# Optimization experiments

Hardware: AMD Instinct MI355X
Metric: run time of the kernel (lower is better)

The kernel has to match this reference:

```python
import jax, jax.numpy as jnp
import numpy as np


def setup_inputs() -> dict:
    key = jax.random.key(0)
    k1, k2, k3, k4, k5 = jax.random.split(key, 5)
    B, N, M, K, D, O = 4, 32768, 8192, 16, 64, 64
    x = jax.random.normal(k1, (B, N, D), jnp.float32)
    x_subset = jax.random.normal(k2, (B, M, D), jnp.float32)
    knn_index = jax.random.randint(k3, (B, M, K), 0, N, jnp.int32)
    # 1x1 Conv2d(2*D -> O) == per-point linear: weight (O, 2D), bias (O,)
    W = jax.random.normal(k4, (O, 2 * D), jnp.float32) * (1.0 / np.sqrt(2 * D))
    b = jax.random.normal(k5, (O,), jnp.float32) * 0.01
    return {"x": x, "x_subset": x_subset, "knn_index": knn_index, "W": W, "b": b}


def reference(x, x_subset, knn_index, W, b):
    # knn_gather: (B,N,D) indexed by (B,M,K) -> (B,M,K,D)
    grouped = jax.vmap(lambda xb, ib: xb[ib])(x, knn_index)
    center = x_subset[:, :, None, :]                      # (B,M,1,D)
    edge = jnp.concatenate(
        [grouped - center, jnp.broadcast_to(center, grouped.shape)], axis=-1
    )                                                     # (B,M,K,2D)
    # 1x1 conv over channel dim + ReLU, output layout (B,O,M,K)
    h = jax.nn.relu(jnp.einsum("bmkc,oc->bomk", edge, W) + b[None, :, None, None])
    return jnp.max(h, axis=-1)                            # (B,O,M)
```

## Files before the change

kernel.cpp:

```cpp
#include <hip/hip_runtime.h>
#include <math.h>

#define B_ 4
#define N_ 32768
#define M_ 8192
#define K_ 16
#define D_ 64
#define O_ 64

typedef __attribute__((ext_vector_type(8))) short bf16x8;
typedef __attribute__((ext_vector_type(4))) float f32x4;

static __device__ __forceinline__ short f2bf(float f) {
    unsigned u = __float_as_uint(f);
    u += 0x7fffu + ((u >> 16) & 1u);
    return (short)(u >> 16);
}

static __device__ __forceinline__ bf16x8 cvt_bf8(float4 f0, float4 f1) {
    bf16x8 v;
    v[0] = f2bf(f0.x); v[1] = f2bf(f0.y); v[2] = f2bf(f0.z); v[3] = f2bf(f0.w);
    v[4] = f2bf(f1.x); v[5] = f2bf(f1.y); v[6] = f2bf(f1.z); v[7] = f2bf(f1.w);
    return v;
}

static __device__ __forceinline__ bf16x8 ld_bf8(const float* p) {
    return cvt_bf8(*(const float4*)p, *(const float4*)(p + 4));
}

__global__ __launch_bounds__(256, 2)
void fused_gconv(const float* __restrict__ x, const float* __restrict__ xs,
                 const int* __restrict__ idx, const float* __restrict__ W,
                 const float* __restrict__ bias, float* __restrict__ out) {
    __shared__ int    ldsI[64 * 16];
    __shared__ bf16x8 ldsW[4][2][2][64];
    __shared__ float  ldsB[64];
    __shared__ float  ldsT[64 * 65];

    const int tid  = threadIdx.x;
    const int blk  = blockIdx.x;
    const int bb   = blk >> 7;
    const int mblk = (blk & 127) * 64;

    *(int4*)&ldsI[tid * 4] =
        *(const int4*)(idx + ((size_t)bb * M_ + mblk) * 16 + tid * 4);

    const int l  = tid & 63;
    const int wv = tid >> 6;
    const int lr = l & 15;
    const int kg = l >> 4;
    const int mw = wv * 16;

    {
        const int t = wv;
        #pragma unroll
        for (int s = 0; s < 2; ++s) {
            const float* wp = W + (size_t)(t * 16 + lr) * 128 + s * 32 + kg * 8;
            float4 f0 = *(const float4*)wp;
            float4 f1 = *(const float4*)(wp + 4);
            float4 g0 = *(const float4*)(wp + 64);
            float4 g1 = *(const float4*)(wp + 68);
            ldsW[t][s][0][l] = cvt_bf8(f0, f1);
            float4 d0 = make_float4(g0.x - f0.x, g0.y - f0.y, g0.z - f0.z, g0.w - f0.w);
            float4 d1 = make_float4(g1.x - f1.x, g1.y - f1.y, g1.z - f1.z, g1.w - f1.w);
            ldsW[t][s][1][l] = cvt_bf8(d0, d1);
        }
        if (tid < 64) ldsB[tid] = bias[tid];
    }
    __syncthreads();

    bf16x8 b1[2][4];
    float  binit[4];
    #pragma unroll
    for (int t = 0; t < 4; ++t) {
        b1[0][t] = ldsW[t][0][0][l];
        b1[1][t] = ldsW[t][1][0][l];
        binit[t] = ldsB[t * 16 + lr];
    }

    const float* xsp = xs + ((size_t)bb * M_ + mblk + mw + lr) * 64 + kg * 8;
    bf16x8 axs0 = ld_bf8(xsp);
    bf16x8 axs1 = ld_bf8(xsp + 32);

    float vout[4][4];
    #pragma unroll
    for (int t = 0; t < 4; ++t) {
        bf16x8 bd0 = ldsW[t][0][1][l];
        bf16x8 bd1 = ldsW[t][1][1][l];
        f32x4 a = {binit[t], binit[t], binit[t], binit[t]};
        a = __builtin_amdgcn_mfma_f32_16x16x32_bf16(axs0, bd0, a, 0, 0, 0);
        a = __builtin_amdgcn_mfma_f32_16x16x32_bf16(axs1, bd1, a, 0, 0, 0);
        vout[t][0] = a[0]; vout[t][1] = a[1];
        vout[t][2] = a[2]; vout[t][3] = a[3];
    }

    int rr[16];
    #pragma unroll
    for (int m = 0; m < 16; ++m)
        rr[m] = ldsI[(mw + m) * 16 + lr];

    const float* xb = x + (size_t)bb * N_ * 64;

    float4 p0[16], p1[16], p2[16], p3[16];
    #pragma unroll
    for (int m = 0; m < 3; ++m) {
        const float* xp = xb + (size_t)(unsigned)rr[m] * 64 + kg * 8;
        p0[m] = *(const float4*)xp;
        p1[m] = *(const float4*)(xp + 4);
        p2[m] = *(const float4*)(xp + 32);
        p3[m] = *(const float4*)(xp + 36);
    }

    #pragma unroll
    for (int m = 0; m < 16; ++m) {
        if (m + 3 < 16) {
            const float* xp = xb + (size_t)(unsigned)rr[m + 3] * 64 + kg * 8;
            p0[m + 3] = *(const float4*)xp;
            p1[m + 3] = *(const float4*)(xp + 4);
            p2[m + 3] = *(const float4*)(xp + 32);
            p3[m + 3] = *(const float4*)(xp + 36);
        }
        bf16x8 a0 = cvt_bf8(p0[m], p1[m]);
        bf16x8 a1 = cvt_bf8(p2[m], p3[m]);
        #pragma unroll
        for (int t = 0; t < 4; ++t) {
            f32x4 a = {0.f, 0.f, 0.f, 0.f};
            a = __builtin_amdgcn_mfma_f32_16x16x32_bf16(a0, b1[0][t], a, 0, 0, 0);
            a = __builtin_amdgcn_mfma_f32_16x16x32_bf16(a1, b1[1][t], a, 0, 0, 0);
            float v = fmaxf(fmaxf(a[0], a[1]), fmaxf(a[2], a[3]));
            v = fmaxf(v, __shfl_xor(v, 16));
            v = fmaxf(v, __shfl_xor(v, 32));
            if ((m >> 2) == kg)
                vout[t][m & 3] += v;
        }
    }

    #pragma unroll
    for (int t = 0; t < 4; ++t)
        #pragma unroll
        for (int r = 0; r < 4; ++r) {
            float v = vout[t][r];
            ldsT[(t * 16 + lr) * 65 + mw + kg * 4 + r] = v > 0.f ? v : 0.f;
        }
    __syncthreads();

    const int o  = tid >> 2;
    const int ms = (tid & 3) * 16;
    float* op = out + ((size_t)bb * 64 + o) * M_ + mblk + ms;
    #pragma unroll
    for (int j = 0; j < 4; ++j) {
        const float* lp = &ldsT[o * 65 + ms + j * 4];
        *(float4*)(op + j * 4) = make_float4(lp[0], lp[1], lp[2], lp[3]);
    }
}

extern "C" void kernel_launch(void* const* d_in, const int* in_sizes, int n_in,
                              void* d_out, int out_size, void* d_ws, size_t ws_size,
                              hipStream_t stream) {
    const float* x    = (const float*)d_in[0];
    const float* xs   = (const float*)d_in[1];
    const int*   idx  = (const int*)d_in[2];
    const float* W    = (const float*)d_in[3];
    const float* bias = (const float*)d_in[4];
    float* out = (float*)d_out;

    fused_gconv<<<(B_ * M_) / 64, 256, 0, stream>>>(x, xs, idx, W, bias, out);
}
```

Before: 28.93 us.

## Split gather work across 8 waves per 32-point block with XCD-aware mapping

Each block now handles 32 centre points with 512 threads, and each wave gathers only 4 points instead of 16. All four neighbour gathers are issued up front and pinned in registers, in place of a 3-deep software pipeline. Block IDs are remapped so that each XCD works on a single batch, which should improve L2 locality for the random gathers of x. The aim is more memory-level parallelism and occupancy for the latency-bound gather. In exchange, the center-term MFMA and weight loads are duplicated across more waves, and the per-wave work is small.

```diff
diff --git a/kernel.cpp b/kernel.cpp
--- a/kernel.cpp
+++ b/kernel.cpp
@@ -28,57 +28,51 @@
     return cvt_bf8(*(const float4*)p, *(const float4*)(p + 4));
 }
 
-__global__ __launch_bounds__(256, 2)
+#define PIN4(q) asm volatile("" :: "v"((q).x), "v"((q).y), "v"((q).z), "v"((q).w))
+
+__global__ __launch_bounds__(512, 4)
 void fused_gconv(const float* __restrict__ x, const float* __restrict__ xs,
                  const int* __restrict__ idx, const float* __restrict__ W,
                  const float* __restrict__ bias, float* __restrict__ out) {
-    __shared__ int    ldsI[64 * 16];
+    __shared__ int    ldsI[512];
     __shared__ bf16x8 ldsW[4][2][2][64];
     __shared__ float  ldsB[64];
-    __shared__ float  ldsT[64 * 65];
+    __shared__ float  ldsT[64 * 33];
 
     const int tid  = threadIdx.x;
     const int blk  = blockIdx.x;
-    const int bb   = blk >> 7;
-    const int mblk = (blk & 127) * 64;
+    const int xcd  = blk & 7;
+    const int slot = blk >> 3;
+    const int bb   = xcd >> 1;
+    const int m0   = (((xcd & 1) << 7) + slot) << 5;
 
-    *(int4*)&ldsI[tid * 4] =
-        *(const int4*)(idx + ((size_t)bb * M_ + mblk) * 16 + tid * 4);
+    ldsI[tid] = idx[((size_t)bb * M_ + m0) * 16 + tid];
 
     const int l  = tid & 63;
     const int wv = tid >> 6;
     const int lr = l & 15;
     const int kg = l >> 4;
-    const int mw = wv * 16;
 
     {
-        const int t = wv;
-        #pragma unroll
-        for (int s = 0; s < 2; ++s) {
-            const float* wp = W + (size_t)(t * 16 + lr) * 128 + s * 32 + kg * 8;
-            float4 f0 = *(const float4*)wp;
-            float4 f1 = *(const float4*)(wp + 4);
-            float4 g0 = *(const float4*)(wp + 64);
-            float4 g1 = *(const float4*)(wp + 68);
-            ldsW[t][s][0][l] = cvt_bf8(f0, f1);
-            float4 d0 = make_float4(g0.x - f0.x, g0.y - f0.y, g0.z - f0.z, g0.w - f0.w);
-            float4 d1 = make_float4(g1.x - f1.x, g1.y - f1.y, g1.z - f1.z, g1.w - f1.w);
-            ldsW[t][s][1][l] = cvt_bf8(d0, d1);
-        }
+        const int t = wv >> 1, s = wv & 1;
+        const float* wp = W + (size_t)(t * 16 + lr) * 128 + s * 32 + kg * 8;
+        float4 f0 = *(const float4*)wp;
+        float4 f1 = *(const float4*)(wp + 4);
+        float4 g0 = *(const float4*)(wp + 64);
+        float4 g1 = *(const float4*)(wp + 68);
+        ldsW[t][s][0][l] = cvt_bf8(f0, f1);
+        float4 d0 = make_float4(g0.x - f0.x, g0.y - f0.y, g0.z - f0.z, g0.w - f0.w);
+        float4 d1 = make_float4(g1.x - f1.x, g1.y - f1.y, g1.z - f1.z, g1.w - f1.w);
+        ldsW[t][s][1][l] = cvt_bf8(d0, d1);
         if (tid < 64) ldsB[tid] = bias[tid];
     }
     __syncthreads();
 
-    bf16x8 b1[2][4];
-    float  binit[4];
+    float binit[4];
     #pragma unroll
-    for (int t = 0; t < 4; ++t) {
-        b1[0][t] = ldsW[t][0][0][l];
-        b1[1][t] = ldsW[t][1][0][l];
-        binit[t] = ldsB[t * 16 + lr];
-    }
+    for (int t = 0; t < 4; ++t) binit[t] = ldsB[t * 16 + lr];
 
-    const float* xsp = xs + ((size_t)bb * M_ + mblk + mw + lr) * 64 + kg * 8;
+    const float* xsp = xs + ((size_t)bb * M_ + m0 + (wv >> 2) * 16 + lr) * 64 + kg * 8;
     bf16x8 axs0 = ld_bf8(xsp);
     bf16x8 axs1 = ld_bf8(xsp + 32);
 
@@ -94,64 +88,75 @@
         vout[t][2] = a[2]; vout[t][3] = a[3];
     }
 
-    int rr[16];
+    int rr[4];
     #pragma unroll
-    for (int m = 0; m < 16; ++m)
-        rr[m] = ldsI[(mw + m) * 16 + lr];
+    for (int j = 0; j < 4; ++j)
+        rr[j] = ldsI[(wv * 4 + j) * 16 + lr];
 
     const float* xb = x + (size_t)bb * N_ * 64;
 
-    float4 p0[16], p1[16], p2[16], p3[16];
+    float4 q0[4], q1[4], q2[4], q3[4];
     #pragma unroll
-    for (int m = 0; m < 3; ++m) {
-        const float* xp = xb + (size_t)(unsigned)rr[m] * 64 + kg * 8;
-        p0[m] = *(const float4*)xp;
-        p1[m] = *(const float4*)(xp + 4);
-        p2[m] = *(const float4*)(xp + 32);
-        p3[m] = *(const float4*)(xp + 36);
+    for (int j = 0; j < 4; ++j) {
+        const float* xp = xb + (size_t)(unsigned)rr[j] * 64 + kg * 8;
+        q0[j] = *(const float4*)xp;
+        q1[j] = *(const float4*)(xp + 4);
+        q2[j] = *(const float4*)(xp + 32);
+        q3[j] = *(const float4*)(xp + 36);
+    }
+    #pragma unroll
+    for (int j = 0; j < 4; ++j) {
+        PIN4(q0[j]); PIN4(q1[j]); PIN4(q2[j]); PIN4(q3[j]);
     }
 
+    bf16x8 a0[4], a1[4];
     #pragma unroll
-    for (int m = 0; m < 16; ++m) {
-        if (m + 3 < 16) {
-            const float* xp = xb + (size_t)(unsigned)rr[m + 3] * 64 + kg * 8;
-            p0[m + 3] = *(const float4*)xp;
-            p1[m + 3] = *(const float4*)(xp + 4);
-            p2[m + 3] = *(const float4*)(xp + 32);
-            p3[m + 3] = *(const float4*)(xp + 36);
-        }
-        bf16x8 a0 = cvt_bf8(p0[m], p1[m]);
-        bf16x8 a1 = cvt_bf8(p2[m], p3[m]);
+    for (int j = 0; j < 4; ++j) {
+        a0[j] = cvt_bf8(q0[j], q1[j]);
+        a1[j] = cvt_bf8(q2[j], q3[j]);
+    }
+
+    float pv[4][4];
+    #pragma unroll
+    for (int t = 0; t < 4; ++t) {
+        bf16x8 w0 = ldsW[t][0][0][l];
+        bf16x8 w1 = ldsW[t][1][0][l];
         #pragma unroll
-        for (int t = 0; t < 4; ++t) {
+        for (int j = 0; j < 4; ++j) {
             f32x4 a = {0.f, 0.f, 0.f, 0.f};
-            a = __builtin_amdgcn_mfma_f32_16x16x32_bf16(a0, b1[0][t], a, 0, 0, 0);
-            a = __builtin_amdgcn_mfma_f32_16x16x32_bf16(a1, b1[1][t], a, 0, 0, 0);
-            float v = fmaxf(fmaxf(a[0], a[1]), fmaxf(a[2], a[3]));
-            v = fmaxf(v, __shfl_xor(v, 16));
-            v = fmaxf(v, __shfl_xor(v, 32));
-            if ((m >> 2) == kg)
-                vout[t][m & 3] += v;
+            a = __builtin_amdgcn_mfma_f32_16x16x32_bf16(a0[j], w0, a, 0, 0, 0);
+            a = __builtin_amdgcn_mfma_f32_16x16x32_bf16(a1[j], w1, a, 0, 0, 0);
+            pv[t][j] = fmaxf(fmaxf(a[0], a[1]), fmaxf(a[2], a[3]));
         }
     }
 
     #pragma unroll
     for (int t = 0; t < 4; ++t)
         #pragma unroll
-        for (int r = 0; r < 4; ++r) {
-            float v = vout[t][r];
-            ldsT[(t * 16 + lr) * 65 + mw + kg * 4 + r] = v > 0.f ? v : 0.f;
+        for (int j = 0; j < 4; ++j) {
+            float v = pv[t][j];
+            v = fmaxf(v, __shfl_xor(v, 16));
+            v = fmaxf(v, __shfl_xor(v, 32));
+            if (kg == (wv & 3))
+                vout[t][j] += v;
         }
+
+    if (kg == (wv & 3)) {
+        #pragma unroll
+        for (int t = 0; t < 4; ++t)
+            #pragma unroll
+            for (int r = 0; r < 4; ++r) {
+                float v = vout[t][r];
+                ldsT[(t * 16 + lr) * 33 + wv * 4 + r] = v > 0.f ? v : 0.f;
+            }
+    }
     __syncthreads();
 
-    const int o  = tid >> 2;
-    const int ms = (tid & 3) * 16;
-    float* op = out + ((size_t)bb * 64 + o) * M_ + mblk + ms;
-    #pragma unroll
-    for (int j = 0; j < 4; ++j) {
-        const float* lp = &ldsT[o * 65 + ms + j * 4];
-        *(float4*)(op + j * 4) = make_float4(lp[0], lp[1], lp[2], lp[3]);
-    }
+    const int o  = tid >> 3;
+    const int ms = (tid & 7) * 4;
+    const float* lp = &ldsT[o * 33 + ms];
+    float4 v = make_float4(lp[0], lp[1], lp[2], lp[3]);
+    *(float4*)(out + ((size_t)bb * 64 + o) * M_ + m0 + ms) = v;
 }
 
 extern "C" void kernel_launch(void* const* d_in, const int* in_sizes, int n_in,
@@ -164,5 +169,5 @@
     const float* bias = (const float*)d_in[4];
     float* out = (float*)d_out;
 
-    fused_gconv<<<(B_ * M_) / 64, 256, 0, stream>>>(x, xs, idx, W, bias, out);
+    fused_gconv<<<(B_ * M_) / 32, 512, 0, stream>>>(x, xs, idx, W, bias, out);
 }
```

Measured after the change: 30.70 us. +6.1%, slower.

## Pre-convert x to bf16 in workspace before the fused gather-conv kernel

Applied to the files above, without the earlier changes.

Adds a separate pass that converts all of x to bf16 in the workspace on every call. The fused kernel then gathers 16-byte bf16 rows directly instead of 32-byte fp32 rows and converting them in-register. This halves the random gather traffic and removes per-use conversion work. In exchange it adds a full streaming read and write of x and a second kernel launch, and it drops the software prefetch pipeline and the occupancy hint in launch_bounds. A slow naive fallback kernel runs if the workspace is too small.

```diff
diff --git a/kernel.cpp b/kernel.cpp
--- a/kernel.cpp
+++ b/kernel.cpp
@@ -28,8 +28,19 @@
     return cvt_bf8(*(const float4*)p, *(const float4*)(p + 4));
 }
 
-__global__ __launch_bounds__(256, 2)
-void fused_gconv(const float* __restrict__ x, const float* __restrict__ xs,
+__global__ __launch_bounds__(256)
+void cvt_x(const float* __restrict__ x, short* __restrict__ xb) {
+    const size_t total = (size_t)B_ * N_ * 64;
+    const size_t stride = (size_t)2048 * 256 * 8;
+    for (size_t i = ((size_t)blockIdx.x * 256 + threadIdx.x) * 8; i < total; i += stride) {
+        float4 f0 = *(const float4*)(x + i);
+        float4 f1 = *(const float4*)(x + i + 4);
+        *(bf16x8*)(xb + i) = cvt_bf8(f0, f1);
+    }
+}
+
+__global__ __launch_bounds__(256)
+void fused_gconv(const short* __restrict__ xb, const float* __restrict__ xs,
                  const int* __restrict__ idx, const float* __restrict__ W,
                  const float* __restrict__ bias, float* __restrict__ out) {
     __shared__ int    ldsI[64 * 16];
@@ -99,29 +110,13 @@
     for (int m = 0; m < 16; ++m)
         rr[m] = ldsI[(mw + m) * 16 + lr];
 
-    const float* xb = x + (size_t)bb * N_ * 64;
-
-    float4 p0[16], p1[16], p2[16], p3[16];
-    #pragma unroll
-    for (int m = 0; m < 3; ++m) {
-        const float* xp = xb + (size_t)(unsigned)rr[m] * 64 + kg * 8;
-        p0[m] = *(const float4*)xp;
-        p1[m] = *(const float4*)(xp + 4);
-        p2[m] = *(const float4*)(xp + 32);
-        p3[m] = *(const float4*)(xp + 36);
-    }
+    const short* xbb = xb + (size_t)bb * N_ * 64;
 
     #pragma unroll
     for (int m = 0; m < 16; ++m) {
-        if (m + 3 < 16) {
-            const float* xp = xb + (size_t)(unsigned)rr[m + 3] * 64 + kg * 8;
-            p0[m + 3] = *(const float4*)xp;
-            p1[m + 3] = *(const float4*)(xp + 4);
-            p2[m + 3] = *(const float4*)(xp + 32);
-            p3[m + 3] = *(const float4*)(xp + 36);
-        }
-        bf16x8 a0 = cvt_bf8(p0[m], p1[m]);
-        bf16x8 a1 = cvt_bf8(p2[m], p3[m]);
+        const short* xp = xbb + (size_t)(unsigned)rr[m] * 64 + kg * 8;
+        bf16x8 a0 = *(const bf16x8*)xp;
+        bf16x8 a1 = *(const bf16x8*)(xp + 32);
         #pragma unroll
         for (int t = 0; t < 4; ++t) {
             f32x4 a = {0.f, 0.f, 0.f, 0.f};
@@ -154,6 +149,30 @@
     }
 }
 
+__global__ void naive_all(const float* __restrict__ x, const float* __restrict__ xs,
+                          const int* __restrict__ idx, const float* __restrict__ W,
+                          const float* __restrict__ bias, float* __restrict__ out) {
+    size_t t = (size_t)blockIdx.x * 256 + threadIdx.x;
+    if (t >= (size_t)B_ * O_ * M_) return;
+    int m = (int)(t % M_);
+    int o = (int)((t / M_) % O_);
+    int b = (int)(t / ((size_t)M_ * O_));
+    const float* xp = x + (size_t)b * N_ * D_;
+    const float* c  = xs + ((size_t)b * M_ + m) * D_;
+    const int*   id = idx + ((size_t)b * M_ + m) * K_;
+    const float* w1 = W + o * 128;
+    const float* w2 = w1 + 64;
+    float best = -INFINITY;
+    for (int k = 0; k < K_; ++k) {
+        const float* g = xp + (size_t)id[k] * D_;
+        float s = bias[o];
+        for (int d = 0; d < D_; ++d)
+            s += (g[d] - c[d]) * w1[d] + c[d] * w2[d];
+        best = fmaxf(best, s);
+    }
+    out[t] = best > 0.0f ? best : 0.0f;
+}
+
 extern "C" void kernel_launch(void* const* d_in, const int* in_sizes, int n_in,
                               void* d_out, int out_size, void* d_ws, size_t ws_size,
                               hipStream_t stream) {
@@ -164,5 +183,15 @@
     const float* bias = (const float*)d_in[4];
     float* out = (float*)d_out;
 
-    fused_gconv<<<(B_ * M_) / 64, 256, 0, stream>>>(x, xs, idx, W, bias, out);
+    const size_t needXB = (size_t)B_ * N_ * 64 * sizeof(short);
+    if (ws_size < needXB) {
+        size_t total = (size_t)B_ * O_ * M_;
+        naive_all<<<(int)((total + 255) / 256), 256, 0, stream>>>(x, xs, idx, W, bias, out);
+        return;
+    }
+
+    short* xb = (short*)d_ws;
+
+    cvt_x<<<2048, 256, 0, stream>>>(x, xb);
+    fused_gconv<<<(B_ * M_) / 64, 256, 0, stream>>>(xb, xs, idx, W, bias, out);
 }
```

Measured after the change: 32.80 us. 13.4% more time.
